# Optimization experiments

Hardware: AMD Instinct MI355X
Metric: run time of the kernel (lower is better)

## Reference

```python
import jax, jax.numpy as jnp
import numpy as np

VOCAB = 3717
PS = 4  # patch_size
AIR_TOKENS = np.array([102, 576, 3352], dtype=np.int32)


def setup_inputs() -> dict:
    key = jax.random.key(0)
    structure = jax.random.randint(key, (32, 32, 32, 32), 0, VOCAB, dtype=jnp.int32)
    return {"structure": structure}


def reference(structure) -> jnp.ndarray:
    B, D, H, W = structure.shape
    nd, nh, nw = D // PS, H // PS, W // PS
    num_patches = nd * nh * nw  # 512
    # [B, nd, PS, nh, PS, nw, PS] -> [B, num_patches, PS^3]
    patches = structure.reshape(B, nd, PS, nh, PS, nw, PS)
    patches = patches.transpose(0, 1, 3, 5, 2, 4, 6).reshape(B * num_patches, PS ** 3)
    P = B * num_patches
    # Per-patch token histogram via scatter-add: [P, VOCAB]
    counts = jnp.zeros((P, VOCAB), dtype=jnp.float32)
    counts = counts.at[jnp.arange(P)[:, None], patches].add(1.0)
    # Drop air tokens from the histogram (equivalent to masking them out of unique/counts)
    counts = counts.at[:, jnp.asarray(AIR_TOKENS)].set(0.0)
    tot = counts.sum(axis=-1)                         # [P]
    probs = counts / jnp.maximum(tot, 1.0)[:, None]   # safe divide; all-air patches -> all zeros
    # zero counts contribute exactly 0*log(1e-10) = 0, matching the unique-values-only sum
    entropy = -(probs * jnp.log(probs + 1e-10)).sum(axis=-1)  # [P]
    total_entropy = entropy.sum()
    return total_entropy / (B * num_patches + 1e-06)
```

## Files before the change

### kernel.cpp

```cpp
#include <hip/hip_runtime.h>


__global__ __launch_bounds__(256) void pcl_k1(const int* __restrict__ s,
                                              float* __restrict__ partial) {
    const int lane = threadIdx.x & 63;
    const int wave = threadIdx.x >> 6;
    const int patch = (blockIdx.x << 2) + wave;

    const int b  = patch >> 9;
    const int pd = (patch >> 6) & 7;
    const int ph = (patch >> 3) & 7;
    const int pw = patch & 7;

    const int ld = lane >> 4;
    const int lh = (lane >> 2) & 3;
    const int lw = lane & 3;

    const int d = (pd << 2) + ld;
    const int h = (ph << 2) + lh;
    const int w = (pw << 2) + lw;
    const int idx = ((b * 32 + d) * 32 + h) * 32 + w;

    const int tok = s[idx];
    const bool air = (tok == 102) | (tok == 576) | (tok == 3352);

    const unsigned long long nb = __ballot(!air);
    const int tot = __popcll(nb);

    int cnt = 0;
    int first = -1;
#pragma unroll
    for (int j = 0; j < 64; ++j) {
        const int t = __shfl(tok, j, 64);
        if (t == tok) {
            ++cnt;
            if (first < 0) first = j;
        }
    }

    float e = 0.0f;
    if (!air && first == lane) {
        const float p = (float)cnt / (float)tot;
        e = -p * __logf(p + 1e-10f);
    }

#pragma unroll
    for (int off = 32; off > 0; off >>= 1) e += __shfl_xor(e, off, 64);

    __shared__ float ws4[4];
    if (lane == 0) ws4[wave] = e;
    __syncthreads();
    if (threadIdx.x == 0)
        partial[blockIdx.x] = ws4[0] + ws4[1] + ws4[2] + ws4[3];
}

__global__ __launch_bounds__(256) void pcl_k2(const float* __restrict__ partial,
                                              float* __restrict__ out, int n) {
    float sum = 0.0f;
    for (int i = threadIdx.x; i < n; i += 256) sum += partial[i];
#pragma unroll
    for (int off = 32; off > 0; off >>= 1) sum += __shfl_xor(sum, off, 64);

    __shared__ float ws4[4];
    const int lane = threadIdx.x & 63;
    const int wave = threadIdx.x >> 6;
    if (lane == 0) ws4[wave] = sum;
    __syncthreads();
    if (threadIdx.x == 0) {
        const float t = ws4[0] + ws4[1] + ws4[2] + ws4[3];
        out[0] = t * (1.0f / (16384.0f + 1e-6f));
    }
}

extern "C" void kernel_launch(void* const* d_in, const int* in_sizes, int n_in,
                              void* d_out, int out_size, void* d_ws, size_t ws_size,
                              hipStream_t stream) {
    const int* s = (const int*)d_in[0];
    float* out = (float*)d_out;
    float* partial = (float*)d_ws;

    pcl_k1<<<4096, 256, 0, stream>>>(s, partial);
    pcl_k2<<<1, 256, 0, stream>>>(partial, out, 4096);
}
```

Baseline: 71.84 us.

## Match equal tokens via bitwise ballots and process four patches per wave

Replaces the 64-step shuffle-compare loop that counts equal tokens with 12 per-bit ballots whose AND gives the mask of lanes holding the same token; the mask's popcount is the count and its lowest set bit marks the first occurrence. Each wave now handles four patches, so the grid shrinks from 4096 to 1024 blocks and the final reduction reads fewer partials. This relies on token values fitting in 12 bits (vocab 3717 < 4096), and the extra per-wave work lowers the number of resident waves available to hide load latency.

```diff
diff --git a/kernel.cpp b/kernel.cpp
--- a/kernel.cpp
+++ b/kernel.cpp
@@ -5,43 +5,39 @@
                                               float* __restrict__ partial) {
     const int lane = threadIdx.x & 63;
     const int wave = threadIdx.x >> 6;
-    const int patch = (blockIdx.x << 2) + wave;
-
-    const int b  = patch >> 9;
-    const int pd = (patch >> 6) & 7;
-    const int ph = (patch >> 3) & 7;
-    const int pw = patch & 7;
+    const int wid = (blockIdx.x << 2) + wave;
 
     const int ld = lane >> 4;
     const int lh = (lane >> 2) & 3;
     const int lw = lane & 3;
 
-    const int d = (pd << 2) + ld;
-    const int h = (ph << 2) + lh;
-    const int w = (pw << 2) + lw;
-    const int idx = ((b * 32 + d) * 32 + h) * 32 + w;
+    float e = 0.0f;
+#pragma unroll
+    for (int it = 0; it < 4; ++it) {
+        const int patch = (wid << 2) + it;
+        const int b  = patch >> 9;
+        const int pd = (patch >> 6) & 7;
+        const int ph = (patch >> 3) & 7;
+        const int pw = patch & 7;
+        const int idx = ((b * 32 + (pd << 2) + ld) * 32 + (ph << 2) + lh) * 32
+                        + (pw << 2) + lw;
 
-    const int tok = s[idx];
-    const bool air = (tok == 102) | (tok == 576) | (tok == 3352);
+        const int tok = s[idx];
+        const bool air = (tok == 102) || (tok == 576) || (tok == 3352);
+        const int tot = __popcll(__ballot(!air));
 
-    const unsigned long long nb = __ballot(!air);
-    const int tot = __popcll(nb);
+        unsigned long long m = ~0ull;
+#pragma unroll
+        for (int bit = 0; bit < 12; ++bit) {
+            const unsigned long long bal = __ballot((tok >> bit) & 1);
+            m &= ((tok >> bit) & 1) ? bal : ~bal;
+        }
 
-    int cnt = 0;
-    int first = -1;
-#pragma unroll
-    for (int j = 0; j < 64; ++j) {
-        const int t = __shfl(tok, j, 64);
-        if (t == tok) {
-            ++cnt;
-            if (first < 0) first = j;
+        const int first = __ffsll((unsigned long long)m) - 1;
+        if (!air && first == lane) {
+            const float p = (float)__popcll(m) / (float)tot;
+            e -= p * __logf(p + 1e-10f);
         }
-    }
-
-    float e = 0.0f;
-    if (!air && first == lane) {
-        const float p = (float)cnt / (float)tot;
-        e = -p * __logf(p + 1e-10f);
     }
 
 #pragma unroll
@@ -79,6 +75,6 @@
     float* out = (float*)d_out;
     float* partial = (float*)d_ws;
 
-    pcl_k1<<<4096, 256, 0, stream>>>(s, partial);
-    pcl_k2<<<1, 256, 0, stream>>>(partial, out, 4096);
+    pcl_k1<<<1024, 256, 0, stream>>>(s, partial);
+    pcl_k2<<<1, 256, 0, stream>>>(partial, out, 1024);
 }
```

Result: faster. 59.82 us (-16.7%).
